# Optimization experiments

Hardware: AMD Instinct MI355X
Metric: run time of the kernel (lower is better)

Reference implementation:

```python
import jax, jax.numpy as jnp
import numpy as np

B, S, D, H = 4, 2048, 1024, 16
DK = D // H

def setup_inputs() -> dict:
    key = jax.random.key(0)
    k1, k2, k3 = jax.random.split(key, 3)
    x = jax.random.normal(k1, (B, S, D), dtype=jnp.float32)
    # kaiming-uniform-ish scale for (d_k, d_model) fan_in = d_model
    bound = 1.0 / np.sqrt(D)
    w_qkv = jax.random.uniform(k2, (3, H, DK, D), dtype=jnp.float32, minval=-bound, maxval=bound)
    w_o = jax.random.uniform(k3, (D, D), dtype=jnp.float32, minval=-bound, maxval=bound)
    return {"x": x, "w_qkv": w_qkv, "w_o": w_o}

def reference(x, w_qkv, w_o):
    seq_len = x.shape[-2]
    d_k = w_qkv.shape[-2]
    # qkv projection: (b s m),(qkv h k m) -> (qkv b h s k)
    qkv = jnp.einsum('bsm,qhkm->qbhsk', x, w_qkv)
    Q, K, V = qkv[0], qkv[1], qkv[2]
    scores = jnp.einsum('bhqk,bhsk->bhqs', Q, K) / jnp.sqrt(jnp.float32(d_k))
    causal = jnp.triu(jnp.ones((seq_len, seq_len), dtype=bool), k=1)
    scores = jnp.where(causal, -jnp.inf, scores)
    probs = jax.nn.softmax(scores, axis=-1)  # (b h s s)
    attn = jnp.einsum('bhqs,bhsk->bhqk', probs, V)
    # concat heads: (b h s k) -> (b s h*k)
    attn = jnp.transpose(attn, (0, 2, 1, 3)).reshape(x.shape[0], seq_len, -1)
    # out proj: y = attn @ w_o.T
    return jnp.einsum('bsd,md->bsm', attn, w_o)
```

## Files before the change

kernel.cpp:

```cpp
#include <hip/hip_runtime.h>
#include <stdint.h>
#include <stddef.h>

typedef unsigned short u16;
typedef float  f32x4  __attribute__((ext_vector_type(4)));
typedef short  s16x8  __attribute__((ext_vector_type(8)));
typedef short  s16x4  __attribute__((ext_vector_type(4)));
typedef __bf16 bf16x8 __attribute__((ext_vector_type(8)));
typedef __bf16 bf16x4 __attribute__((ext_vector_type(4)));
typedef u16    u16x4  __attribute__((ext_vector_type(4)));

#define DEV static __device__ __forceinline__

DEV u16 f2bf(float f){
  uint32_t u = __builtin_bit_cast(uint32_t, f);
  u += 0x7FFFu + ((u >> 16) & 1u);
  return (u16)(u >> 16);
}

DEV f32x4 mfma16(s16x8 a, s16x8 b, f32x4 c){
  return __builtin_amdgcn_mfma_f32_16x16x32_bf16(
      __builtin_bit_cast(bf16x8, a), __builtin_bit_cast(bf16x8, b), c, 0, 0, 0);
}

DEV f32x4 mfma16k(s16x4 a, s16x4 b, f32x4 c){
  return __builtin_amdgcn_mfma_f32_16x16x16bf16_1k(a, b, c, 0, 0, 0);
}

DEV float exp2_fast(float x){ return __builtin_exp2f(x); }

DEV void gl_lds16(const u16* g, u16* l){
  __builtin_amdgcn_global_load_lds(
      (__attribute__((address_space(1))) void*)(g),
      (__attribute__((address_space(3))) void*)(l), 16, 0, 0);
}

__global__ __launch_bounds__(256) void cvt_all(const float* __restrict__ x,
                                               const float* __restrict__ wqkv,
                                               const float* __restrict__ wo,
                                               u16* __restrict__ outb){
  const int N1 = 2097152;
  const int N2 = N1 + 786432;
  const int NT = N2 + 262144;
  const int stride = gridDim.x * blockDim.x;
  for (int i = blockIdx.x * blockDim.x + threadIdx.x; i < NT; i += stride){
    const float* src; int j;
    if (i < N1){ src = x; j = i; }
    else if (i < N2){ src = wqkv; j = i - N1; }
    else { src = wo; j = i - N2; }
    float4 v = *(const float4*)(src + (size_t)j * 4);
    u16x4 o = { f2bf(v.x), f2bf(v.y), f2bf(v.z), f2bf(v.w) };
    *(u16x4*)(outb + (size_t)i * 4) = o;
  }
}

DEV void gemm_core(const u16* __restrict__ A, const u16* __restrict__ Bw,
                   int K, int bm, int bn, u16* ldsA, u16* ldsB, f32x4 acc[4][4])
{
  const int lane = threadIdx.x & 63;
  const int wave = threadIdx.x >> 6;
  const int wm = (wave >> 1) * 64, wn = (wave & 1) * 64;
  const int l8 = (lane & 7) * 8;
  const int lr = lane >> 3;
  const int fr = lane & 15;
  const int k8 = (lane >> 4) * 8;

  #pragma unroll
  for (int m = 0; m < 4; m++)
    #pragma unroll
    for (int n = 0; n < 4; n++){ f32x4 z = {0.f,0.f,0.f,0.f}; acc[m][n] = z; }

  const int nkt = K >> 6;
  for (int kt = 0; kt < nkt; ++kt){
    const int kb = kt * 64;
    #pragma unroll
    for (int i = 0; i < 4; i++){
      const int c   = wave * 4 + i;
      const int row = c * 8 + lr;
      gl_lds16(A  + (size_t)(bm + row) * K + kb + l8, ldsA + c * 512);
      gl_lds16(Bw + (size_t)(bn + row) * K + kb + l8, ldsB + c * 512);
    }
    __syncthreads();
    #pragma unroll
    for (int kk = 0; kk < 2; ++kk){
      s16x8 af[4], bfr[4];
      #pragma unroll
      for (int m = 0; m < 4; m++) af[m]  = *(const s16x8*)(ldsA + (wm + m*16 + fr)*64 + kk*32 + k8);
      #pragma unroll
      for (int n = 0; n < 4; n++) bfr[n] = *(const s16x8*)(ldsB + (wn + n*16 + fr)*64 + kk*32 + k8);
      #pragma unroll
      for (int m = 0; m < 4; m++)
        #pragma unroll
        for (int n = 0; n < 4; n++)
          acc[m][n] = mfma16(af[m], bfr[n], acc[m][n]);
    }
    __syncthreads();
  }
}

__global__ __launch_bounds__(256) void gemm_qkv(const u16* __restrict__ xb,
                                                const u16* __restrict__ wb,
                                                u16* __restrict__ Qd,
                                                u16* __restrict__ Kd,
                                                u16* __restrict__ Vtd)
{
  __shared__ __align__(16) u16 ldsA[128*64];
  __shared__ __align__(16) u16 ldsB[128*64];
  f32x4 acc[4][4];
  const int bm = blockIdx.x * 128, bn = blockIdx.y * 128;
  gemm_core(xb, wb, 1024, bm, bn, ldsA, ldsB, acc);

  const int lane = threadIdx.x & 63, wave = threadIdx.x >> 6;
  const int wm = (wave >> 1) * 64, wn = (wave & 1) * 64;
  const int fr = lane & 15, r4 = (lane >> 4) * 4;
  const int q = bn >> 10;

  #pragma unroll
  for (int m = 0; m < 4; m++){
    const int i0 = bm + wm + m*16 + r4;
    const int b  = i0 >> 11;
    const int s0 = i0 & 2047;
    #pragma unroll
    for (int n = 0; n < 4; n++){
      const int ng = bn + wn + n*16 + fr;
      const int h  = (ng >> 6) & 15, kd = ng & 63;
      const size_t bh = (size_t)(b * 16 + h);
      if (q == 0){
        #pragma unroll
        for (int r = 0; r < 4; r++)
          Qd[(bh*2048 + s0 + r)*64 + kd] = f2bf(acc[m][n][r] * 0.18033688011112042f);
      } else if (q == 1){
        #pragma unroll
        for (int r = 0; r < 4; r++)
          Kd[(bh*2048 + s0 + r)*64 + kd] = f2bf(acc[m][n][r]);
      } else {
        u16x4 v = { f2bf(acc[m][n][0]), f2bf(acc[m][n][1]),
                    f2bf(acc[m][n][2]), f2bf(acc[m][n][3]) };
        *(u16x4*)(Vtd + (bh*64 + kd)*2048 + s0) = v;
      }
    }
  }
}

__global__ __launch_bounds__(256) void gemm_outp(const u16* __restrict__ attnb,
                                                 const u16* __restrict__ wob,
                                                 float* __restrict__ C)
{
  __shared__ __align__(16) u16 ldsA[128*64];
  __shared__ __align__(16) u16 ldsB[128*64];
  f32x4 acc[4][4];
  const int bm = blockIdx.x * 128, bn = blockIdx.y * 128;
  gemm_core(attnb, wob, 1024, bm, bn, ldsA, ldsB, acc);

  const int lane = threadIdx.x & 63, wave = threadIdx.x >> 6;
  const int wm = (wave >> 1) * 64, wn = (wave & 1) * 64;
  const int fr = lane & 15, r4 = (lane >> 4) * 4;
  #pragma unroll
  for (int m = 0; m < 4; m++){
    const int i0 = bm + wm + m*16 + r4;
    #pragma unroll
    for (int n = 0; n < 4; n++){
      const int ng = bn + wn + n*16 + fr;
      #pragma unroll
      for (int r = 0; r < 4; r++)
        C[(size_t)(i0 + r) * 1024 + ng] = acc[m][n][r];
    }
  }
}

DEV void chunk_step1(const u16* Kc, const u16* Vc, int kb, int q0,
                     const s16x8 (&qf)[2], f32x4 (&O)[4], f32x4 &L,
                     float &mrun, s16x4 ones,
                     int fr, int g, int f, int r4)
{
  f32x4 sc[4];
  #pragma unroll
  for (int mi = 0; mi < 4; mi++){ f32x4 z = {0.f,0.f,0.f,0.f}; sc[mi] = z; }
  __builtin_amdgcn_s_setprio(1);
  #pragma unroll
  for (int kk = 0; kk < 2; kk++)
    #pragma unroll
    for (int mi = 0; mi < 4; mi++){
      s16x8 kf = *(const s16x8*)(Kc + (mi*16 + fr)*64 + ((kk*4 + g) ^ f)*8);
      sc[mi] = mfma16(kf, qf[kk], sc[mi]);
    }
  __builtin_amdgcn_s_setprio(0);

  const int q_g = q0 + fr;
  float tmax = -1e30f;
  if (kb + 63 > q0){
    #pragma unroll
    for (int mi = 0; mi < 4; mi++)
      #pragma unroll
      for (int r = 0; r < 4; r++){
        const int s_g = kb + mi*16 + r4 + r;
        float v = sc[mi][r];
        v = (s_g > q_g) ? -1e30f : v;
        sc[mi][r] = v;
        tmax = fmaxf(tmax, v);
      }
  } else {
    #pragma unroll
    for (int mi = 0; mi < 4; mi++)
      #pragma unroll
      for (int r = 0; r < 4; r++)
        tmax = fmaxf(tmax, sc[mi][r]);
  }
  float m_new = mrun;
  if (!__all(tmax <= m_new + 8.f)){
    float tm = fmaxf(tmax, __shfl_xor(tmax, 16));
    tm = fmaxf(tm, __shfl_xor(tm, 32));
    m_new = fmaxf(m_new, tm);
    const float corr = exp2_fast(mrun - m_new);
    mrun = m_new;
    L[0] *= corr;
    #pragma unroll
    for (int n = 0; n < 4; n++)
      #pragma unroll
      for (int r = 0; r < 4; r++)
        O[n][r] *= corr;
  }
  s16x4 pb[4];
  #pragma unroll
  for (int mi = 0; mi < 4; mi++){
    f32x4 e;
    #pragma unroll
    for (int r = 0; r < 4; r++)
      e[r] = exp2_fast(sc[mi][r] - m_new);
    pb[mi] = __builtin_bit_cast(s16x4, __builtin_convertvector(e, bf16x4));
  }

  __builtin_amdgcn_s_setprio(1);
  #pragma unroll
  for (int mi = 0; mi < 4; mi++){
    L = mfma16k(ones, pb[mi], L);
    #pragma unroll
    for (int n = 0; n < 4; n++){
      s16x4 vf = *(const s16x4*)(Vc + (n*16 + fr)*64 + ((2*mi + (g >> 1)) ^ f)*8 + (g & 1)*4);
      O[n] = mfma16k(vf, pb[mi], O[n]);
    }
  }
  __builtin_amdgcn_s_setprio(0);
}

__global__ __launch_bounds__(256, 4) void attn_fwd(const u16* __restrict__ Qd,
                                                   const u16* __restrict__ Kd,
                                                   const u16* __restrict__ Vtd,
                                                   u16* __restrict__ attnb)
{
  __shared__ __align__(16) u16 Kl[2][64*64];
  __shared__ __align__(16) u16 Vl[2][64*64];

  const int t = threadIdx.x;
  const int lane = t & 63, w = t >> 6;
  const int wg = blockIdx.x;
  const int bh = 8 * (wg & 7) + (wg >> 7);
  const int ph = (wg >> 3) & 15;
  const int p  = ph >> 1, half = ph & 1;
  const int qh = 8 + p, ql = 7 - p;
  const u16* Qp = Qd  + (size_t)bh * 2048 * 64;
  const u16* Kp = Kd  + (size_t)bh * 2048 * 64;
  const u16* Vp = Vtd + (size_t)bh * 64 * 2048;

  const int fr = lane & 15, g = lane >> 4;
  const int f  = fr & 7;
  const int k8 = g * 8, r4 = g * 4;
  const int rgs = half * 4 + w;
  const int qh0 = qh * 128 + rgs * 16;
  const int ql0 = ql * 128 + rgs * 16;
  const int nkt = 2 * qh + 2;

  const s16x4 ones = { 0x3F80, 0x3F80, 0x3F80, 0x3F80 };

  s16x8 qfh[2], qfl[2];
  #pragma unroll
  for (int kk = 0; kk < 2; kk++){
    qfh[kk] = *(const s16x8*)(Qp + (size_t)(qh0 + fr) * 64 + kk*32 + k8);
    qfl[kk] = *(const s16x8*)(Qp + (size_t)(ql0 + fr) * 64 + kk*32 + k8);
  }

  f32x4 Ohi[4], Olo[4], Lhi, Llo;
  #pragma unroll
  for (int n = 0; n < 4; n++){
    f32x4 z = {0.f,0.f,0.f,0.f}; Ohi[n] = z; Olo[n] = z;
  }
  { f32x4 z = {0.f,0.f,0.f,0.f}; Lhi = z; Llo = z; }
  float mh = -1e30f, ml = -1e30f;

  const int Lr  = t >> 3;
  const int cs8 = ((t & 7) ^ (Lr & 7)) * 8;
  const u16* kS = Kp + Lr * 64 + cs8;
  const u16* vS = Vp + (size_t)Lr * 2048 + cs8;

  gl_lds16(kS,         (u16*)Kl + t*8);
  gl_lds16(kS + 2048,  (u16*)Kl + t*8 + 2048);
  gl_lds16(vS,         (u16*)Vl + t*8);
  gl_lds16(vS + 65536, (u16*)Vl + t*8 + 2048);
  kS += 4096; vS += 64;

  for (int kt = 0; kt < nkt; ++kt){
    __syncthreads();
    const int cur = kt & 1;
    if (kt + 1 < nkt){
      u16* kD = (u16*)Kl + (cur ^ 1) * 4096 + t*8;
      u16* vD = (u16*)Vl + (cur ^ 1) * 4096 + t*8;
      gl_lds16(kS,         kD);
      gl_lds16(kS + 2048,  kD + 2048);
      gl_lds16(vS,         vD);
      gl_lds16(vS + 65536, vD + 2048);
    }
    kS += 4096; vS += 64;

    const int kb = kt * 64;
    const u16* Kc = Kl[cur];
    const u16* Vc = Vl[cur];

    if (kb <= qh0 + 15)
      chunk_step1(Kc, Vc, kb, qh0, qfh, Ohi, Lhi, mh, ones, fr, g, f, r4);
    if (kb <= ql0 + 15)
      chunk_step1(Kc, Vc, kb, ql0, qfl, Olo, Llo, ml, ones, fr, g, f, r4);
  }

  const int b = bh >> 4, h = bh & 15;
  const float invh = 1.0f / Lhi[0];
  const float invl = 1.0f / Llo[0];
  const int sh = qh0 + fr;
  const int sl = ql0 + fr;
  #pragma unroll
  for (int n = 0; n < 4; n++){
    u16x4 vh = { f2bf(Ohi[n][0]*invh), f2bf(Ohi[n][1]*invh),
                 f2bf(Ohi[n][2]*invh), f2bf(Ohi[n][3]*invh) };
    *(u16x4*)(attnb + (((size_t)b*2048 + sh)*16 + h)*64 + n*16 + r4) = vh;
    u16x4 vl = { f2bf(Olo[n][0]*invl), f2bf(Olo[n][1]*invl),
                 f2bf(Olo[n][2]*invl), f2bf(Olo[n][3]*invl) };
    *(u16x4*)(attnb + (((size_t)b*2048 + sl)*16 + h)*64 + n*16 + r4) = vl;
  }
}

extern "C" void kernel_launch(void* const* d_in, const int* in_sizes, int n_in,
                              void* d_out, int out_size, void* d_ws, size_t ws_size,
                              hipStream_t stream)
{
  const float* x    = (const float*)d_in[0];
  const float* wqkv = (const float*)d_in[1];
  const float* wo   = (const float*)d_in[2];
  float* out = (float*)d_out;

  char* ws = (char*)d_ws;
  u16* xb    = (u16*)(ws);
  u16* wqb   = (u16*)(ws + 16777216);
  u16* wob   = (u16*)(ws + 23068672);
  u16* Qd    = (u16*)(ws + 25165824);
  u16* Kd    = (u16*)(ws + 41943040);
  u16* Vtd   = (u16*)(ws + 58720256);
  u16* attnb = xb;

  cvt_all<<<3072, 256, 0, stream>>>(x, wqkv, wo, xb);
  gemm_qkv<<<dim3(64, 24), 256, 0, stream>>>(xb, wqb, Qd, Kd, Vtd);
  attn_fwd<<<dim3(1024), 256, 0, stream>>>(Qd, Kd, Vtd, attnb);
  gemm_outp<<<dim3(64, 8), 256, 0, stream>>>(attnb, wob, out);
}
```

Measured before the change: 200.3 us.

## Double-buffer LDS tiles in GEMM core to overlap global loads with MFMA

```diff
diff --git a/kernel.cpp b/kernel.cpp
--- a/kernel.cpp
+++ b/kernel.cpp
@@ -60,8 +60,6 @@
   const int lane = threadIdx.x & 63;
   const int wave = threadIdx.x >> 6;
   const int wm = (wave >> 1) * 64, wn = (wave & 1) * 64;
-  const int l8 = (lane & 7) * 8;
-  const int lr = lane >> 3;
   const int fr = lane & 15;
   const int k8 = (lane >> 4) * 8;
 
@@ -70,31 +68,45 @@
     #pragma unroll
     for (int n = 0; n < 4; n++){ f32x4 z = {0.f,0.f,0.f,0.f}; acc[m][n] = z; }
 
+  const int c0 = wave * 4;
+  const u16* aS = A  + (size_t)(bm + c0*8 + (lane >> 3)) * K + (lane & 7) * 8;
+  const u16* bS = Bw + (size_t)(bn + c0*8 + (lane & 7) * 0 + (lane >> 3)) * K + (lane & 7) * 8;
+
+  #pragma unroll
+  for (int i = 0; i < 4; i++){
+    gl_lds16(aS + (size_t)i*8*K, ldsA + (c0 + i) * 512);
+    gl_lds16(bS + (size_t)i*8*K, ldsB + (c0 + i) * 512);
+  }
+
   const int nkt = K >> 6;
+  int cur = 0;
   for (int kt = 0; kt < nkt; ++kt){
-    const int kb = kt * 64;
-    #pragma unroll
-    for (int i = 0; i < 4; i++){
-      const int c   = wave * 4 + i;
-      const int row = c * 8 + lr;
-      gl_lds16(A  + (size_t)(bm + row) * K + kb + l8, ldsA + c * 512);
-      gl_lds16(Bw + (size_t)(bn + row) * K + kb + l8, ldsB + c * 512);
-    }
     __syncthreads();
+    if (kt + 1 < nkt){
+      const int kb2 = (kt + 1) << 6;
+      const int nb  = (cur ^ 1) * 8192;
+      #pragma unroll
+      for (int i = 0; i < 4; i++){
+        gl_lds16(aS + (size_t)i*8*K + kb2, ldsA + nb + (c0 + i) * 512);
+        gl_lds16(bS + (size_t)i*8*K + kb2, ldsB + nb + (c0 + i) * 512);
+      }
+    }
+    const u16* As = ldsA + cur * 8192;
+    const u16* Bs = ldsB + cur * 8192;
     #pragma unroll
     for (int kk = 0; kk < 2; ++kk){
       s16x8 af[4], bfr[4];
       #pragma unroll
-      for (int m = 0; m < 4; m++) af[m]  = *(const s16x8*)(ldsA + (wm + m*16 + fr)*64 + kk*32 + k8);
-      #pragma unroll
-      for (int n = 0; n < 4; n++) bfr[n] = *(const s16x8*)(ldsB + (wn + n*16 + fr)*64 + kk*32 + k8);
+      for (int m = 0; m < 4; m++) af[m]  = *(const s16x8*)(As + (wm + m*16 + fr)*64 + kk*32 + k8);
+      #pragma unroll
+      for (int n = 0; n < 4; n++) bfr[n] = *(const s16x8*)(Bs + (wn + n*16 + fr)*64 + kk*32 + k8);
       #pragma unroll
       for (int m = 0; m < 4; m++)
         #pragma unroll
         for (int n = 0; n < 4; n++)
           acc[m][n] = mfma16(af[m], bfr[n], acc[m][n]);
     }
-    __syncthreads();
+    cur ^= 1;
   }
 }
 
@@ -104,8 +116,8 @@
                                                 u16* __restrict__ Kd,
                                                 u16* __restrict__ Vtd)
 {
-  __shared__ __align__(16) u16 ldsA[128*64];
-  __shared__ __align__(16) u16 ldsB[128*64];
+  __shared__ __align__(16) u16 ldsA[2*128*64];
+  __shared__ __align__(16) u16 ldsB[2*128*64];
   f32x4 acc[4][4];
   const int bm = blockIdx.x * 128, bn = blockIdx.y * 128;
   gemm_core(xb, wb, 1024, bm, bn, ldsA, ldsB, acc);
@@ -146,8 +158,8 @@
                                                  const u16* __restrict__ wob,
                                                  float* __restrict__ C)
 {
-  __shared__ __align__(16) u16 ldsA[128*64];
-  __shared__ __align__(16) u16 ldsB[128*64];
+  __shared__ __align__(16) u16 ldsA[2*128*64];
+  __shared__ __align__(16) u16 ldsB[2*128*64];
   f32x4 acc[4][4];
   const int bm = blockIdx.x * 128, bn = blockIdx.y * 128;
   gemm_core(attnb, wob, 1024, bm, bn, ldsA, ldsB, acc);
```

After: 211.5 us. +5.6%, slower.
